# Kernel optimization log

Hardware: AMD Instinct MI355X
Metric: run time of the kernel (lower is better)

Reference implementation:

```python
import jax, jax.numpy as jnp
import numpy as np

N_NODES = 100000
N_EDGES = 1600000
D_H = 64
D_E = 64
D_Q = 64
D_HID = 128
N_GRAPHS = 16


def _mlp_params(key, d_in, d_hid):
    k1, k2, k3, k4 = jax.random.split(key, 4)
    s1 = 1.0 / np.sqrt(d_in)
    s2 = 1.0 / np.sqrt(d_hid)
    return (
        jax.random.uniform(k1, (d_in, d_hid), jnp.float32, -s1, s1),
        jax.random.uniform(k2, (d_hid,), jnp.float32, -s1, s1),
        jax.random.uniform(k3, (d_hid, 1), jnp.float32, -s2, s2),
        jax.random.uniform(k4, (1,), jnp.float32, -s2, s2),
    )


def setup_inputs() -> dict:
    key = jax.random.key(0)
    ks = jax.random.split(key, 8)
    h = jax.random.normal(ks[0], (N_NODES, D_H), jnp.float32)
    e = jax.random.normal(ks[1], (N_EDGES, D_E), jnp.float32)
    q = jax.random.normal(ks[2], (N_GRAPHS, D_Q), jnp.float32)
    edge_index = jax.random.randint(ks[3], (2, N_EDGES), 0, N_NODES, jnp.int64)
    edge_batch = jax.random.randint(ks[4], (N_EDGES,), 0, N_GRAPHS, jnp.int64)
    gw1, gb1, gw2, gb2 = _mlp_params(ks[5], 2 * D_H + D_Q, D_HID)
    sw1, sb1, sw2, sb2 = _mlp_params(ks[6], 2 * D_H + D_E, D_HID)
    return {
        "h": h, "e": e, "q": q,
        "edge_index": edge_index, "edge_batch": edge_batch,
        "gate_w1": gw1, "gate_b1": gb1, "gate_w2": gw2, "gate_b2": gb2,
        "score_w1": sw1, "score_b1": sb1, "score_w2": sw2, "score_b2": sb2,
    }


def _mlp(x, w1, b1, w2, b2):
    # 2-layer MLP, no layernorm (use_layer_norm=False), output dim 1
    hidden = jax.nn.relu(x @ w1 + b1)
    return (hidden @ w2 + b2)[..., 0]


def _dst_softmax(raw, dst, num_nodes):
    # numerically stable per-destination softmax via segment reductions
    max_vals = jax.ops.segment_max(raw, dst, num_segments=num_nodes)
    exp_vals = jnp.exp(raw - max_vals[dst])
    sum_exp = jax.ops.segment_sum(exp_vals, dst, num_segments=num_nodes)
    denom = jnp.maximum(sum_exp[dst], 1e-9)
    return exp_vals / denom


def reference(h, e, q, edge_index, edge_batch,
              gate_w1, gate_b1, gate_w2, gate_b2,
              score_w1, score_b1, score_w2, score_b2):
    src, dst = edge_index[0], edge_index[1]
    h_i = h[src]            # [E, d_h]
    h_j = h[dst]            # [E, d_h]
    q_e = q[edge_batch]     # [E, d_q]
    gate_in = jnp.concatenate([h_i, h_j, q_e], axis=-1)
    gate = jax.nn.sigmoid(_mlp(gate_in, gate_w1, gate_b1, gate_w2, gate_b2))
    score_in = jnp.concatenate([h_i, h_j, e], axis=-1)
    score = _mlp(score_in, score_w1, score_b1, score_w2, score_b2)
    raw = gate * score
    return _dst_softmax(raw, dst, h.shape[0])
```

## Files before the change

kernel.cpp:

```cpp
#include <hip/hip_runtime.h>
#include <hip/hip_bf16.h>

#define NN 100000
#define NE 1600000

typedef __attribute__((ext_vector_type(8))) unsigned short ushort8v;
typedef __attribute__((ext_vector_type(4))) unsigned short ushort4v;
typedef __attribute__((ext_vector_type(8))) short short8v;
typedef __attribute__((ext_vector_type(4))) float f32x4;

__device__ __forceinline__ float b2f(unsigned short u) {
  return __uint_as_float(((unsigned)u) << 16);
}
__device__ __forceinline__ short f2bs(float f) {
  unsigned u = __float_as_uint(f);
  unsigned r = (u + 0x7FFFu + ((u >> 16) & 1u)) >> 16;
  return (short)r;
}

__global__ void qproj_kernel(const float* __restrict__ q,
                             const float* __restrict__ gw1,
                             const float* __restrict__ gb1,
                             float* __restrict__ Qg) {
  int g = blockIdx.x, j = threadIdx.x;
  float acc = gb1[j];
  for (int k = 0; k < 64; ++k) acc += q[g * 64 + k] * gw1[(128 + k) * 128 + j];
  Qg[g * 128 + j] = acc;
}

__global__ __launch_bounds__(1024) void prepack_kernel(
    const float* __restrict__ sw1, short8v* __restrict__ WtG) {
  int tid = threadIdx.x;
  int t = tid >> 7, ks = (tid >> 6) & 1, lane = tid & 63;
  int qg = lane >> 4, cl = lane & 15;
  short8v fr;
#pragma unroll
  for (int j = 0; j < 8; ++j)
    fr[j] = f2bs(sw1[(128 + ks * 32 + qg * 8 + j) * 128 + t * 16 + cl]);
  WtG[tid] = fr;
}

__global__ __launch_bounds__(256) void nodeproj_kernel(
    const float* __restrict__ h, const float* __restrict__ gw1,
    const float* __restrict__ sw1, __hip_bfloat16* __restrict__ GA,
    __hip_bfloat16* __restrict__ GB, __hip_bfloat16* __restrict__ SA,
    __hip_bfloat16* __restrict__ SB) {
  __shared__ float hs[64][64];
  __shared__ float Ws[64][128];
  int part = blockIdx.y;
  const float* W = (part & 1) ? sw1 : gw1;
  int roff = (part >= 2) ? 64 : 0;
  __hip_bfloat16* outp = (part == 0) ? GA : (part == 1) ? SA : (part == 2) ? GB : SB;
  int n0 = blockIdx.x * 64;
  int t = threadIdx.x;

  {
    int n = t & 63, kc = t >> 6;
    int gn = n0 + n;
#pragma unroll
    for (int i = 0; i < 4; ++i) {
      int k = kc * 16 + i * 4;
      float4 hv = make_float4(0.f, 0.f, 0.f, 0.f);
      if (gn < NN) hv = *(const float4*)&h[gn * 64 + k];
      hs[k + 0][n] = hv.x; hs[k + 1][n] = hv.y;
      hs[k + 2][n] = hv.z; hs[k + 3][n] = hv.w;
    }
  }
  {
    const float* Wb = W + roff * 128;
    float* wsf = &Ws[0][0];
#pragma unroll
    for (int i = 0; i < 8; ++i) {
      int flat = (i * 256 + t) * 4;
      *(float4*)&wsf[flat] = *(const float4*)&Wb[flat];
    }
  }
  __syncthreads();

  int tx = t & 31, ty = t >> 5;
  float acc[8][4] = {};
#pragma unroll 4
  for (int k = 0; k < 64; ++k) {
    float hn[8];
    *(float4*)&hn[0] = *(const float4*)&hs[k][ty * 8];
    *(float4*)&hn[4] = *(const float4*)&hs[k][ty * 8 + 4];
    float wv[4];
#pragma unroll
    for (int i = 0; i < 4; ++i) wv[i] = Ws[k][tx + 32 * i];
#pragma unroll
    for (int j = 0; j < 8; ++j)
#pragma unroll
      for (int i = 0; i < 4; ++i) acc[j][i] += hn[j] * wv[i];
  }
#pragma unroll
  for (int j = 0; j < 8; ++j) {
    int gn = n0 + ty * 8 + j;
    if (gn < NN) {
#pragma unroll
      for (int i = 0; i < 4; ++i)
        outp[(size_t)gn * 128 + tx + 32 * i] = __float2bfloat16(acc[j][i]);
    }
  }
}

__global__ __launch_bounds__(256) void edge_kernel(
    const float* __restrict__ e, const int* __restrict__ eidx,
    const int* __restrict__ ebat,
    const __hip_bfloat16* __restrict__ GA, const __hip_bfloat16* __restrict__ GB,
    const __hip_bfloat16* __restrict__ SA, const __hip_bfloat16* __restrict__ SB,
    const float* __restrict__ Qg, const short8v* __restrict__ WtG,
    const float* __restrict__ sb1, const float* __restrict__ gw2,
    const float* __restrict__ gb2, const float* __restrict__ sw2,
    const float* __restrict__ sb2, float* __restrict__ out,
    float* __restrict__ nsum) {
  __shared__ short8v WtS[1024];
  __shared__ f32x4 QgS[16 * 33];
  __shared__ f32x4 gw2S[32], sb1S[32], sw2S[32];
  const int tid = threadIdx.x;
  const int w = tid >> 6, lane = tid & 63;
  const int qg = lane >> 4, cl = lane & 15;
  const int EB = blockIdx.x * 256 + w * 64;
  const unsigned short* GAU = (const unsigned short*)GA;
  const unsigned short* GBU = (const unsigned short*)GB;
  const unsigned short* SAU = (const unsigned short*)SA;
  const unsigned short* SBU = (const unsigned short*)SB;
  const float sb2v = sb2[0], gb2v = gb2[0];

  int srcv = eidx[EB + cl];
  int dstv = eidx[NE + EB + cl];
  int gv   = ebat[EB + cl];

  {
    const f32x4* s4 = (const f32x4*)WtG;
    f32x4* d4 = (f32x4*)WtS;
#pragma unroll
    for (int i = 0; i < 4; ++i) d4[tid + i * 256] = s4[tid + i * 256];
    const f32x4* q4 = (const f32x4*)Qg;
    QgS[(tid >> 5) * 33 + (tid & 31)] = q4[tid];
    {
      int t2 = tid + 256;
      QgS[(t2 >> 5) * 33 + (t2 & 31)] = q4[t2];
    }
    if (tid < 32) {
      gw2S[tid] = ((const f32x4*)gw2)[tid];
      sb1S[tid] = ((const f32x4*)sb1)[tid];
      sw2S[tid] = ((const f32x4*)sw2)[tid];
    }
  }
  __syncthreads();

#pragma unroll 1
  for (int rt = 0; rt < 4; ++rt) {
    const int erow = EB + rt * 16 + cl;

    const float* ap = e + (size_t)erow * 64 + qg * 8;
    f32x4 f0 = __builtin_nontemporal_load((const f32x4*)(ap + 0));
    f32x4 f1 = __builtin_nontemporal_load((const f32x4*)(ap + 4));
    f32x4 f2 = __builtin_nontemporal_load((const f32x4*)(ap + 32));
    f32x4 f3 = __builtin_nontemporal_load((const f32x4*)(ap + 36));

    const unsigned short* gr = GAU + (size_t)srcv * 128 + qg * 32;
    const unsigned short* hr = GBU + (size_t)dstv * 128 + qg * 32;
    ushort8v gav[4], gbv[4];
#pragma unroll
    for (int c = 0; c < 4; ++c) {
      gav[c] = *(const ushort8v*)(gr + c * 8);
      gbv[c] = *(const ushort8v*)(hr + c * 8);
    }
    const unsigned short* sr = SAU + (size_t)srcv * 128 + qg * 4;
    const unsigned short* dr = SBU + (size_t)dstv * 128 + qg * 4;
    ushort4v sav[8], sbv[8];
#pragma unroll
    for (int t = 0; t < 8; ++t) {
      sav[t] = *(const ushort4v*)(sr + t * 16);
      sbv[t] = *(const ushort4v*)(dr + t * 16);
    }

    int srcn = srcv, dstn = dstv, gn = gv;
    if (rt < 3) {
      int er2 = erow + 16;
      srcn = eidx[er2];
      dstn = eidx[NE + er2];
      gn   = ebat[er2];
    }

    short8v b0, b1;
    b0[0] = f2bs(f0.x); b0[1] = f2bs(f0.y); b0[2] = f2bs(f0.z); b0[3] = f2bs(f0.w);
    b0[4] = f2bs(f1.x); b0[5] = f2bs(f1.y); b0[6] = f2bs(f1.z); b0[7] = f2bs(f1.w);
    b1[0] = f2bs(f2.x); b1[1] = f2bs(f2.y); b1[2] = f2bs(f2.z); b1[3] = f2bs(f2.w);
    b1[4] = f2bs(f3.x); b1[5] = f2bs(f3.y); b1[6] = f2bs(f3.z); b1[7] = f2bs(f3.w);

    float gpart = 0.f;
#pragma unroll
    for (int c = 0; c < 4; ++c) {
      ushort8v av = gav[c], bv = gbv[c];
      f32x4 q0 = QgS[gv * 33 + qg * 8 + c * 2];
      f32x4 q1 = QgS[gv * 33 + qg * 8 + c * 2 + 1];
      f32x4 w0 = gw2S[qg * 8 + c * 2];
      f32x4 w1 = gw2S[qg * 8 + c * 2 + 1];
#pragma unroll
      for (int ii = 0; ii < 4; ++ii) {
        float x = b2f(av[ii]) + b2f(bv[ii]) + q0[ii];
        gpart = fmaf(fmaxf(x, 0.f), w0[ii], gpart);
      }
#pragma unroll
      for (int ii = 0; ii < 4; ++ii) {
        float x = b2f(av[4 + ii]) + b2f(bv[4 + ii]) + q1[ii];
        gpart = fmaf(fmaxf(x, 0.f), w1[ii], gpart);
      }
    }

    float part = 0.f;
#pragma unroll
    for (int t = 0; t < 8; ++t) {
      short8v Aw0 = WtS[(t * 2 + 0) * 64 + lane];
      short8v Aw1 = WtS[(t * 2 + 1) * 64 + lane];
      f32x4 acc = (f32x4){0.f, 0.f, 0.f, 0.f};
      acc = __builtin_amdgcn_mfma_f32_16x16x32_bf16(Aw0, b0, acc, 0, 0, 0);
      acc = __builtin_amdgcn_mfma_f32_16x16x32_bf16(Aw1, b1, acc, 0, 0, 0);
      f32x4 bb = sb1S[t * 4 + qg];
      f32x4 ww = sw2S[t * 4 + qg];
#pragma unroll
      for (int i = 0; i < 4; ++i) {
        float sx = acc[i] + b2f(sav[t][i]) + b2f(sbv[t][i]) + bb[i];
        part = fmaf(fmaxf(sx, 0.f), ww[i], part);
      }
    }

    part += __shfl_xor(part, 16, 64);
    part += __shfl_xor(part, 32, 64);
    gpart += __shfl_xor(gpart, 16, 64);
    gpart += __shfl_xor(gpart, 32, 64);
    if (lane < 16) {
      int E = EB + rt * 16 + cl;
      float gate = 1.f / (1.f + __expf(-(gpart + gb2v)));
      float ex = __expf(gate * (part + sb2v));
      out[E] = ex;
      atomicAdd(&nsum[dstv], ex);
    }
    srcv = srcn; dstv = dstn; gv = gn;
  }
}

__global__ __launch_bounds__(256) void norm_kernel(
    const int* __restrict__ eidx, const float* __restrict__ nodesum,
    float* __restrict__ out) {
  int ee = blockIdx.x * 256 + threadIdx.x;
  int dst = eidx[NE + ee];
  out[ee] = out[ee] / fmaxf(nodesum[dst], 1e-9f);
}

extern "C" void kernel_launch(void* const* d_in, const int* in_sizes, int n_in,
                              void* d_out, int out_size, void* d_ws, size_t ws_size,
                              hipStream_t stream) {
  const float* h   = (const float*)d_in[0];
  const float* e   = (const float*)d_in[1];
  const float* q   = (const float*)d_in[2];
  const int* eidx  = (const int*)d_in[3];
  const int* ebat  = (const int*)d_in[4];
  const float* gw1 = (const float*)d_in[5];
  const float* gb1 = (const float*)d_in[6];
  const float* gw2 = (const float*)d_in[7];
  const float* gb2 = (const float*)d_in[8];
  const float* sw1 = (const float*)d_in[9];
  const float* sb1 = (const float*)d_in[10];
  const float* sw2 = (const float*)d_in[11];
  const float* sb2 = (const float*)d_in[12];
  float* out = (float*)d_out;

  char* ws = (char*)d_ws;
  __hip_bfloat16* GA = (__hip_bfloat16*)ws;
  __hip_bfloat16* GB = (__hip_bfloat16*)(ws + 25600000);
  __hip_bfloat16* SA = (__hip_bfloat16*)(ws + 51200000);
  __hip_bfloat16* SB = (__hip_bfloat16*)(ws + 76800000);
  float* Qg    = (float*)(ws + 102400000);
  short8v* WtG = (short8v*)(ws + 102400000 + 8192);
  float* nsum  = (float*)(ws + 102400000 + 8192 + 16384);

  (void)hipMemsetAsync(nsum, 0, 400000, stream);
  qproj_kernel<<<dim3(16), dim3(128), 0, stream>>>(q, gw1, gb1, Qg);
  prepack_kernel<<<dim3(1), dim3(1024), 0, stream>>>(sw1, WtG);
  nodeproj_kernel<<<dim3(1563, 4), dim3(256), 0, stream>>>(h, gw1, sw1, GA, GB, SA, SB);
  edge_kernel<<<dim3(NE / 256), dim3(256), 0, stream>>>(
      e, eidx, ebat, GA, GB, SA, SB, Qg, WtG, sb1, gw2, gb2, sw2, sb2, out, nsum);
  norm_kernel<<<dim3(NE / 256), dim3(256), 0, stream>>>(eidx, nsum, out);
}
```

Measured before the change: 529.8 us.

## Interleave gate and score node projections into one contiguous row per node

Merges the separate gate and score projection tables into combined 256-wide bf16 rows per source and destination node. The columns are permuted so each lane's gate and score values sit in one contiguous 128-byte chunk, with matching permutations in the weight prepack and the bias/weight indexing. This turns the scattered 8-byte gathers into 16-byte vector loads from a single cache-friendly region per node, cutting gather transactions in the memory-bound edge kernel. It also adds an occupancy hint to launch bounds, which may constrain register allocation.

Result: slower. 1.181 ms (+122.9%).

```diff
diff --git a/kernel.cpp b/kernel.cpp
--- a/kernel.cpp
+++ b/kernel.cpp
@@ -5,7 +5,6 @@
 #define NE 1600000
 
 typedef __attribute__((ext_vector_type(8))) unsigned short ushort8v;
-typedef __attribute__((ext_vector_type(4))) unsigned short ushort4v;
 typedef __attribute__((ext_vector_type(8))) short short8v;
 typedef __attribute__((ext_vector_type(4))) float f32x4;
 
@@ -33,24 +32,25 @@
   int tid = threadIdx.x;
   int t = tid >> 7, ks = (tid >> 6) & 1, lane = tid & 63;
   int qg = lane >> 4, cl = lane & 15;
+  int d = 32 * (cl >> 2) + 4 * t + (cl & 3);
   short8v fr;
 #pragma unroll
   for (int j = 0; j < 8; ++j)
-    fr[j] = f2bs(sw1[(128 + ks * 32 + qg * 8 + j) * 128 + t * 16 + cl]);
+    fr[j] = f2bs(sw1[(128 + ks * 32 + qg * 8 + j) * 128 + d]);
   WtG[tid] = fr;
 }
 
 __global__ __launch_bounds__(256) void nodeproj_kernel(
     const float* __restrict__ h, const float* __restrict__ gw1,
-    const float* __restrict__ sw1, __hip_bfloat16* __restrict__ GA,
-    __hip_bfloat16* __restrict__ GB, __hip_bfloat16* __restrict__ SA,
-    __hip_bfloat16* __restrict__ SB) {
+    const float* __restrict__ sw1, __hip_bfloat16* __restrict__ SRCP,
+    __hip_bfloat16* __restrict__ DSTP) {
   __shared__ float hs[64][64];
   __shared__ float Ws[64][128];
   int part = blockIdx.y;
   const float* W = (part & 1) ? sw1 : gw1;
   int roff = (part >= 2) ? 64 : 0;
-  __hip_bfloat16* outp = (part == 0) ? GA : (part == 1) ? SA : (part == 2) ? GB : SB;
+  __hip_bfloat16* outp = (part >= 2) ? DSTP : SRCP;
+  int goff = (part & 1) ? 32 : 0;
   int n0 = blockIdx.x * 64;
   int t = threadIdx.x;
 
@@ -98,16 +98,15 @@
     if (gn < NN) {
 #pragma unroll
       for (int i = 0; i < 4; ++i)
-        outp[(size_t)gn * 128 + tx + 32 * i] = __float2bfloat16(acc[j][i]);
-    }
-  }
-}
-
-__global__ __launch_bounds__(256) void edge_kernel(
+        outp[(size_t)gn * 256 + i * 64 + goff + tx] = __float2bfloat16(acc[j][i]);
+    }
+  }
+}
+
+__global__ __launch_bounds__(256, 4) void edge_kernel(
     const float* __restrict__ e, const int* __restrict__ eidx,
     const int* __restrict__ ebat,
-    const __hip_bfloat16* __restrict__ GA, const __hip_bfloat16* __restrict__ GB,
-    const __hip_bfloat16* __restrict__ SA, const __hip_bfloat16* __restrict__ SB,
+    const __hip_bfloat16* __restrict__ SRCP, const __hip_bfloat16* __restrict__ DSTP,
     const float* __restrict__ Qg, const short8v* __restrict__ WtG,
     const float* __restrict__ sb1, const float* __restrict__ gw2,
     const float* __restrict__ gb2, const float* __restrict__ sw2,
@@ -120,10 +119,8 @@
   const int w = tid >> 6, lane = tid & 63;
   const int qg = lane >> 4, cl = lane & 15;
   const int EB = blockIdx.x * 256 + w * 64;
-  const unsigned short* GAU = (const unsigned short*)GA;
-  const unsigned short* GBU = (const unsigned short*)GB;
-  const unsigned short* SAU = (const unsigned short*)SA;
-  const unsigned short* SBU = (const unsigned short*)SB;
+  const unsigned short* SU = (const unsigned short*)SRCP;
+  const unsigned short* DU = (const unsigned short*)DSTP;
   const float sb2v = sb2[0], gb2v = gb2[0];
 
   int srcv = eidx[EB + cl];
@@ -159,21 +156,15 @@
     f32x4 f2 = __builtin_nontemporal_load((const f32x4*)(ap + 32));
     f32x4 f3 = __builtin_nontemporal_load((const f32x4*)(ap + 36));
 
-    const unsigned short* gr = GAU + (size_t)srcv * 128 + qg * 32;
-    const unsigned short* hr = GBU + (size_t)dstv * 128 + qg * 32;
-    ushort8v gav[4], gbv[4];
+    const ushort8v* sp = (const ushort8v*)(SU + (size_t)srcv * 256 + qg * 64);
+    const ushort8v* dp = (const ushort8v*)(DU + (size_t)dstv * 256 + qg * 64);
+    ushort8v gav[4], gbv[4], sav[4], sbv[4];
 #pragma unroll
     for (int c = 0; c < 4; ++c) {
-      gav[c] = *(const ushort8v*)(gr + c * 8);
-      gbv[c] = *(const ushort8v*)(hr + c * 8);
-    }
-    const unsigned short* sr = SAU + (size_t)srcv * 128 + qg * 4;
-    const unsigned short* dr = SBU + (size_t)dstv * 128 + qg * 4;
-    ushort4v sav[8], sbv[8];
-#pragma unroll
-    for (int t = 0; t < 8; ++t) {
-      sav[t] = *(const ushort4v*)(sr + t * 16);
-      sbv[t] = *(const ushort4v*)(dr + t * 16);
+      gav[c] = sp[c];
+      gbv[c] = dp[c];
+      sav[c] = sp[4 + c];
+      sbv[c] = dp[4 + c];
     }
 
     int srcn = srcv, dstn = dstv, gn = gv;
@@ -218,11 +209,12 @@
       f32x4 acc = (f32x4){0.f, 0.f, 0.f, 0.f};
       acc = __builtin_amdgcn_mfma_f32_16x16x32_bf16(Aw0, b0, acc, 0, 0, 0);
       acc = __builtin_amdgcn_mfma_f32_16x16x32_bf16(Aw1, b1, acc, 0, 0, 0);
-      f32x4 bb = sb1S[t * 4 + qg];
-      f32x4 ww = sw2S[t * 4 + qg];
+      f32x4 bb = sb1S[qg * 8 + t];
+      f32x4 ww = sw2S[qg * 8 + t];
 #pragma unroll
       for (int i = 0; i < 4; ++i) {
-        float sx = acc[i] + b2f(sav[t][i]) + b2f(sbv[t][i]) + bb[i];
+        float sx = acc[i] + b2f(sav[t >> 1][(t & 1) * 4 + i]) +
+                   b2f(sbv[t >> 1][(t & 1) * 4 + i]) + bb[i];
         part = fmaf(fmaxf(sx, 0.f), ww[i], part);
       }
     }
@@ -269,10 +261,8 @@
   float* out = (float*)d_out;
 
   char* ws = (char*)d_ws;
-  __hip_bfloat16* GA = (__hip_bfloat16*)ws;
-  __hip_bfloat16* GB = (__hip_bfloat16*)(ws + 25600000);
-  __hip_bfloat16* SA = (__hip_bfloat16*)(ws + 51200000);
-  __hip_bfloat16* SB = (__hip_bfloat16*)(ws + 76800000);
+  __hip_bfloat16* SRCP = (__hip_bfloat16*)ws;
+  __hip_bfloat16* DSTP = (__hip_bfloat16*)(ws + 51200000);
   float* Qg    = (float*)(ws + 102400000);
   short8v* WtG = (short8v*)(ws + 102400000 + 8192);
   float* nsum  = (float*)(ws + 102400000 + 8192 + 16384);
@@ -280,8 +270,8 @@
   (void)hipMemsetAsync(nsum, 0, 400000, stream);
   qproj_kernel<<<dim3(16), dim3(128), 0, stream>>>(q, gw1, gb1, Qg);
   prepack_kernel<<<dim3(1), dim3(1024), 0, stream>>>(sw1, WtG);
-  nodeproj_kernel<<<dim3(1563, 4), dim3(256), 0, stream>>>(h, gw1, sw1, GA, GB, SA, SB);
+  nodeproj_kernel<<<dim3(1563, 4), dim3(256), 0, stream>>>(h, gw1, sw1, SRCP, DSTP);
   edge_kernel<<<dim3(NE / 256), dim3(256), 0, stream>>>(
-      e, eidx, ebat, GA, GB, SA, SB, Qg, WtG, sb1, gw2, gb2, sw2, sb2, out, nsum);
+      e, eidx, ebat, SRCP, DSTP, Qg, WtG, sb1, gw2, gb2, sw2, sb2, out, nsum);
   norm_kernel<<<dim3(NE / 256), dim3(256), 0, stream>>>(eidx, nsum, out);
 }
```
